# Performance work log

Hardware: AMD Instinct MI355X
Metric: run time of the kernel (lower is better)

Reference implementation:

```python
import jax, jax.numpy as jnp
import numpy as np

B, T, C = 2, 2048, 2048
H, HD = 16, 128          # n_head, head_dim
D_C, D_C1, D_ROPE = 512, 512, 64
D_NOPE = HD - D_ROPE     # 64
M = 4                    # move_slots
EPS = 1.1920929e-07      # torch fp32 rms_norm default eps


def _rope(x, cos, sin):
    # x: (B,T,h,D), cos/sin: (B,T,D//2) -> broadcast over head axis
    c = cos[:, :, None, :]
    s = sin[:, :, None, :]
    x1, x2 = jnp.split(x, 2, axis=-1)
    return jnp.concatenate([x1 * c + x2 * s, -x1 * s + x2 * c], axis=-1)


def _rmsnorm(x):
    return x * jax.lax.rsqrt(jnp.mean(x * x, axis=-1, keepdims=True) + EPS)


def setup_inputs() -> dict:
    key = jax.random.key(0)
    ks = jax.random.split(key, 8)
    # realistic decoupled-RoPE angles over d_rope//2 frequencies
    inv_freq = 1.0 / (10000.0 ** (np.arange(0, D_ROPE, 2) / D_ROPE))  # (32,)
    ang = np.arange(T)[:, None] * inv_freq[None, :]                   # (T,32)
    cos = jnp.broadcast_to(jnp.cos(ang)[None].astype(jnp.float32), (B, T, D_ROPE // 2))
    sin = jnp.broadcast_to(jnp.sin(ang)[None].astype(jnp.float32), (B, T, D_ROPE // 2))
    return {
        "x": jax.random.normal(ks[0], (B, T, C), jnp.float32),
        "ve": jax.random.normal(ks[1], (B, T, M * H * HD), jnp.float32),
        "cos": cos,
        "sin": sin,
        "w_down": jax.random.normal(ks[2], (C, D_C + D_C1 + D_ROPE), jnp.float32) * 0.02,
        "w_ukv": jax.random.normal(ks[3], (D_C, H * (D_NOPE + HD)), jnp.float32) * 0.02,
        "w_uq": jax.random.normal(ks[4], (D_C1, H * HD), jnp.float32) * 0.02,
        "w_gate": jax.random.normal(ks[5], (C, H * (M + 1)), jnp.float32) * 0.02,
        "w_proj": jax.random.normal(ks[6], (H * HD, C), jnp.float32) * 0.02,
        "window_size": 2048,
    }


def reference(x, ve, cos, sin, w_down, w_ukv, w_uq, w_gate, w_proj, window_size):
    # fused down projection, split into kv-latent / q-latent / rope part
    down = x @ w_down                                          # (B,T,1088)
    c_kv, c_q, k_rope_raw = jnp.split(down, [D_C, D_C + D_C1], axis=-1)

    kv = (c_kv @ w_ukv).reshape(B, T, H, D_NOPE + HD)
    k_nope, v = jnp.split(kv, [D_NOPE], axis=-1)               # (B,T,H,64), (B,T,H,128)

    k_rope = _rope(k_rope_raw.reshape(B, T, 1, D_ROPE), cos, sin)  # (B,T,1,64)

    # MoVE gating: per-head gate on v plus mixture over M value-embedding slots
    ve5 = ve.reshape(B, T, M, H, HD)
    gates = 2.0 * jax.nn.sigmoid(x @ w_gate).reshape(B, T, H, M + 1)
    v = gates[..., 0:1] * v + jnp.einsum('bthm,btmhd->bthd', gates[..., 1:], ve5)

    q = (c_q @ w_uq).reshape(B, T, H, HD)
    q_nope, q_rope = jnp.split(q, [D_NOPE], axis=-1)
    q_rope = _rope(q_rope, cos, sin)

    k = jnp.concatenate([k_nope, jnp.broadcast_to(k_rope, (B, T, H, D_ROPE))], axis=-1)
    q = jnp.concatenate([q_nope, q_rope], axis=-1)
    q, k = _rmsnorm(q), _rmsnorm(k)

    # sliding-window causal attention (flash_attn semantics: j<=i and i-j<=window)
    scale = 1.0 / float(np.sqrt(HD))
    scores = jnp.einsum('bthd,bshd->bhts', q, k) * scale       # (B,H,T,T)
    i = jnp.arange(T)[:, None]
    j = jnp.arange(T)[None, :]
    mask = (j <= i) & ((i - j) <= window_size)
    scores = jnp.where(mask, scores, -jnp.inf)
    attn = jax.nn.softmax(scores, axis=-1)
    y = jnp.einsum('bhts,bshd->bthd', attn, v)                 # (B,T,H,HD)

    return y.reshape(B, T, H * HD) @ w_proj                    # (B,T,C)
```

## Files before the change

kernel.cpp:

```cpp
#include <hip/hip_runtime.h>

typedef unsigned short u16;
typedef __bf16 bfv8 __attribute__((ext_vector_type(8)));
typedef float f32x4 __attribute__((ext_vector_type(4)));
typedef u16 u16x8 __attribute__((ext_vector_type(8)));

#define B_      2
#define T_      2048
#define C_      2048
#define H_      16
#define HD_     128
#define NT_     (B_ * T_)
#define DOWN_N  1088
#define DCAT    1168
#define DCATP   1280
#define KV_N    3072
#define Q_N     2048
#define EPS_    1.1920929e-07f
#define CEXP    0.12751879524580262f
#define SMAXS   16.6f

__device__ __forceinline__ float b2f(u16 u) {
    union { unsigned u; float f; } c; c.u = ((unsigned)u) << 16; return c.f;
}
__device__ __forceinline__ u16 f2b(float f) {
    union { float f; unsigned u; } c; c.f = f;
    return (u16)((c.u + 0x7FFFu + ((c.u >> 16) & 1u)) >> 16);
}
__device__ __forceinline__ float dynload(const void* p, size_t i, int bf) {
    if (bf) return b2f(((const u16*)p)[i]);
    return ((const float*)p)[i];
}

__device__ __forceinline__ void gload16(const u16* g, u16* l) {
    __builtin_amdgcn_global_load_lds(
        (const __attribute__((address_space(1))) void*)g,
        (__attribute__((address_space(3))) void*)l,
        16, 0, 0);
}

__global__ void detect_kernel(const unsigned* __restrict__ x, int* __restrict__ flag) {
    __shared__ int cnt;
    if (threadIdx.x == 0) cnt = 0;
    __syncthreads();
    int c = 0;
    for (int i = threadIdx.x; i < 4096; i += 256) {
        const unsigned w = x[i];
        const unsigned e = (w >> 7) & 0xFF;
        if (e >= 105 && e <= 140) ++c;
    }
    atomicAdd(&cnt, c);
    __syncthreads();
    if (threadIdx.x == 0) flag[0] = (cnt > 2300) ? 1 : 0;
}

__global__ __launch_bounds__(256) void cast_kernel(
    const void* __restrict__ in, u16* __restrict__ out, int n, const int* __restrict__ flagp)
{
    const int fl = flagp[0];
    const int i0 = (blockIdx.x * 256 + threadIdx.x) * 8;
    if (i0 + 8 > n) return;
    u16x8 o;
    #pragma unroll
    for (int i = 0; i < 8; ++i) o[i] = f2b(dynload(in, (size_t)i0 + i, fl));
    *(u16x8*)(out + i0) = o;
}

__global__ __launch_bounds__(256) void tcast_kernel(
    const void* __restrict__ in, u16* __restrict__ out, int K, int N, int Ntot,
    const int* __restrict__ flagp)
{
    const int fl = flagp[0];
    __shared__ float sf[32][33];
    const int n0 = blockIdx.x * 32, k0 = blockIdx.y * 32;
    const int tx = threadIdx.x & 31, ty = threadIdx.x >> 5;
    const int cr = (n0 + tx < N) ? (n0 + tx) : (N - 1);
    #pragma unroll
    for (int i = 0; i < 4; ++i)
        sf[ty + 8 * i][tx] = dynload(in, (size_t)(k0 + ty + 8 * i) * N + cr, fl);
    __syncthreads();
    #pragma unroll
    for (int i = 0; i < 4; ++i) {
        const int n = n0 + ty + 8 * i;
        if (n < Ntot) out[(size_t)n * K + k0 + tx] = (n < N) ? f2b(sf[tx][ty + 8 * i]) : (u16)0;
    }
}

__device__ __forceinline__ void stc(u16* p, float v)  { *p = f2b(v); }
__device__ __forceinline__ void stc(float* p, float v){ *p = v; }

template <typename TC>
__global__ __launch_bounds__(256) void mfma_gemm(
    const u16* __restrict__ A, int lda,
    const u16* __restrict__ BT, int ldb,
    TC* __restrict__ Cm, int ldc,
    int M, int N, int K)
{
    __shared__ u16 As[128 * 32];
    __shared__ u16 Bs[128 * 32];
    const int tid = threadIdx.x;
    const int m0 = blockIdx.y * 128, n0 = blockIdx.x * 128;
    const int w = tid >> 6, l = tid & 63;
    const int wm = (w >> 1) * 64, wn = (w & 1) * 64;
    const int lr = l & 15, lq = l >> 4;

    f32x4 acc[4][4];
    #pragma unroll
    for (int i = 0; i < 4; ++i)
        #pragma unroll
        for (int j = 0; j < 4; ++j) acc[i][j] = (f32x4){0.f, 0.f, 0.f, 0.f};

    const int srow = w * 32 + (l >> 2);
    const int scol = (l & 3) * 8;
    const u16* ag = A  + (size_t)(m0 + srow) * lda + scol;
    const u16* bg = BT + (size_t)(n0 + srow) * ldb + scol;
    u16* as0 = &As[(w * 32) * 32];
    u16* as1 = &As[(w * 32 + 16) * 32];
    u16* bs0 = &Bs[(w * 32) * 32];
    u16* bs1 = &Bs[(w * 32 + 16) * 32];

    for (int k0 = 0; k0 < K; k0 += 32) {
        gload16(ag + k0,            as0);
        gload16(ag + 16 * lda + k0, as1);
        gload16(bg + k0,            bs0);
        gload16(bg + 16 * ldb + k0, bs1);
        __syncthreads();
        bfv8 af[4], bf[4];
        #pragma unroll
        for (int mi = 0; mi < 4; ++mi) af[mi] = *(const bfv8*)&As[(wm + mi * 16 + lr) * 32 + lq * 8];
        #pragma unroll
        for (int ni = 0; ni < 4; ++ni) bf[ni] = *(const bfv8*)&Bs[(wn + ni * 16 + lr) * 32 + lq * 8];
        #pragma unroll
        for (int mi = 0; mi < 4; ++mi)
            #pragma unroll
            for (int ni = 0; ni < 4; ++ni)
                acc[mi][ni] = __builtin_amdgcn_mfma_f32_16x16x32_bf16(af[mi], bf[ni], acc[mi][ni], 0, 0, 0);
        __syncthreads();
    }

    #pragma unroll
    for (int mi = 0; mi < 4; ++mi) {
        #pragma unroll
        for (int ni = 0; ni < 4; ++ni) {
            const int col = n0 + wn + ni * 16 + lr;
            if (col < N) {
                #pragma unroll
                for (int r = 0; r < 4; ++r) {
                    const int row = m0 + wm + mi * 16 + lq * 4 + r;
                    stc(&Cm[(size_t)row * ldc + col], acc[mi][ni][r]);
                }
            }
        }
    }
}

__global__ __launch_bounds__(256) void assemble_kernel(
    const u16* __restrict__ down,
    const u16* __restrict__ qraw,
    const u16* __restrict__ kv,
    const void* __restrict__ ve,
    const void* __restrict__ cosg,
    const void* __restrict__ sing,
    u16* __restrict__ qo, u16* __restrict__ ko, u16* __restrict__ vo,
    const int* __restrict__ flagp)
{
    const int fl = flagp[0];
    const int bt = blockIdx.x;
    const int tid = threadIdx.x;
    __shared__ float cs[32], sn[32], kr[64];
    if (tid < 32) {
        cs[tid] = dynload(cosg, (size_t)bt * 32 + tid, fl);
        sn[tid] = dynload(sing, (size_t)bt * 32 + tid, fl);
    }
    __syncthreads();
    if (tid < 64) {
        const u16* rp = down + (size_t)bt * DCAT + 1024;
        const int d = tid;
        if (d < 32) kr[d] = b2f(rp[d]) * cs[d] + b2f(rp[d + 32]) * sn[d];
        else { const int r = d - 32; kr[d] = -b2f(rp[d - 32]) * sn[r] + b2f(rp[d]) * cs[r]; }
    }
    __syncthreads();

    const int h = tid >> 4;
    const int lane = tid & 15;
    const int d0 = lane * 8;

    const u16* qr = qraw + (size_t)bt * Q_N + h * HD_;
    float vq[8];
    float ss = 0.f;
    #pragma unroll
    for (int i = 0; i < 8; ++i) {
        const int d = d0 + i;
        float xv = b2f(qr[d]);
        if (d >= 64) {
            if (d < 96) { const int r = d - 64; xv = xv * cs[r] + b2f(qr[d + 32]) * sn[r]; }
            else        { const int r = d - 96; xv = -b2f(qr[d - 32]) * sn[r] + xv * cs[r]; }
        }
        vq[i] = xv; ss += xv * xv;
    }
    #pragma unroll
    for (int off = 1; off < 16; off <<= 1) ss += __shfl_xor(ss, off);
    float rms = rsqrtf(ss * (1.f / 128.f) + EPS_);
    u16* qop = qo + (size_t)bt * Q_N + h * HD_ + d0;
    #pragma unroll
    for (int i = 0; i < 8; ++i) qop[i] = f2b(vq[i] * rms);

    const u16* kvp = kv + (size_t)bt * KV_N + h * 192;
    float vk[8];
    ss = 0.f;
    #pragma unroll
    for (int i = 0; i < 8; ++i) {
        const int d = d0 + i;
        const float xv = (d < 64) ? b2f(kvp[d]) : kr[d - 64];
        vk[i] = xv; ss += xv * xv;
    }
    #pragma unroll
    for (int off = 1; off < 16; off <<= 1) ss += __shfl_xor(ss, off);
    rms = rsqrtf(ss * (1.f / 128.f) + EPS_);
    u16* kop = ko + (size_t)bt * Q_N + h * HD_ + d0;
    #pragma unroll
    for (int i = 0; i < 8; ++i) kop[i] = f2b(vk[i] * rms);

    float g[5];
    #pragma unroll
    for (int j = 0; j < 5; ++j) {
        const float logit = b2f(down[(size_t)bt * DCAT + 1088 + h * 5 + j]);
        g[j] = 2.f / (1.f + expf(-logit));
    }
    const u16* vp = kvp + 64;
    const size_t vebase = (size_t)bt * 8192 + h * HD_;
    u16* vop = vo + (size_t)bt * Q_N + h * HD_ + d0;
    #pragma unroll
    for (int i = 0; i < 8; ++i) {
        const int d = d0 + i;
        float val = g[0] * b2f(vp[d]);
        #pragma unroll
        for (int m = 0; m < 4; ++m) val += g[1 + m] * dynload(ve, vebase + m * 2048 + d, fl);
        vop[i] = f2b(val);
    }
}

__global__ __launch_bounds__(256) void vtrans_kernel(
    const u16* __restrict__ vn, u16* __restrict__ vt)
{
    __shared__ u16 s[64][72];
    const int t0 = blockIdx.x * 64;
    const int d0 = blockIdx.y * 64;
    const int bh = blockIdx.z;
    const int tid = threadIdx.x;
    {
        const int tt = tid >> 2, seg = tid & 3;
        const u16* p = vn + ((size_t)((bh >> 4) * T_) + t0 + tt) * 2048 + (bh & 15) * 128 + d0 + seg * 16;
        u16x8 v0 = *(const u16x8*)(p);
        u16x8 v1 = *(const u16x8*)(p + 8);
        *(u16x8*)&s[tt][seg * 16]     = v0;
        *(u16x8*)&s[tt][seg * 16 + 8] = v1;
    }
    __syncthreads();
    {
        const int dd = tid >> 2, tseg = tid & 3;
        u16* q = vt + ((size_t)(bh * 128) + d0 + dd) * T_ + t0 + tseg * 16;
        #pragma unroll
        for (int g = 0; g < 2; ++g) {
            u16x8 o;
            #pragma unroll
            for (int i = 0; i < 8; ++i) o[i] = s[tseg * 16 + g * 8 + i][dd];
            *(u16x8*)(q + g * 8) = o;
        }
    }
}

__global__ __launch_bounds__(256) void attn_mfma(
    const u16* __restrict__ qn, const u16* __restrict__ kn,
    const u16* __restrict__ vt, u16* __restrict__ yb,
    const int* __restrict__ wptr)
{
    __shared__ u16 Ks[64][136];
    __shared__ u16 VTs[144][72];
    __shared__ u16 Ps[4][32][72];

    const int flat = (int)(blockIdx.x + (blockIdx.y << 4) + (blockIdx.z << 8));
    const int b  = flat & 1;
    const int h  = ((flat >> 1) & 7) | ((flat >> 5) & 8);
    const int q4 = (flat >> 4) & 15;
    const int mb = ((flat ^ (flat >> 8)) & 1) ? (q4 ^ 15) : q4;
    const int m0 = mb * 128;
    const int W = wptr[0];
    const int tid = threadIdx.x;
    const int w = tid >> 6, l = tid & 63;
    const int lr = l & 15, lq = l >> 4;
    const int qr0 = m0 + w * 32;

    bfv8 qf[2][4];
    #pragma unroll
    for (int mi = 0; mi < 2; ++mi) {
        const u16* qp = qn + ((size_t)(b * T_) + qr0 + mi * 16 + lr) * 2048 + h * 128 + lq * 8;
        #pragma unroll
        for (int kk = 0; kk < 4; ++kk) qf[mi][kk] = *(const bfv8*)(qp + kk * 32);
    }

    f32x4 oacc[2][8];
    f32x4 lacc[2];
    #pragma unroll
    for (int mi = 0; mi < 2; ++mi) {
        lacc[mi] = (f32x4){0.f, 0.f, 0.f, 0.f};
        #pragma unroll
        for (int od = 0; od < 8; ++od) oacc[mi][od] = (f32x4){0.f, 0.f, 0.f, 0.f};
    }

    {
        const int rr = 128 + (tid >> 4), cc = (tid & 15) * 4;
        const u16 v = (tid >> 4) == 0 ? (u16)0x3F80 : (u16)0;
        VTs[rr][cc] = v; VTs[rr][cc + 1] = v; VTs[rr][cc + 2] = v; VTs[rr][cc + 3] = v;
    }

    const int kkey = tid >> 2, kq = tid & 3;
    const int vd = tid >> 1, vh2 = tid & 1;

    int ns = m0 - W; if (ns < 0) ns = 0; ns &= ~63;
    const int ne = m0 + 64;

    const u16* kbase = kn + ((size_t)(b * T_) + kkey) * 2048 + h * 128 + kq * 32;
    const u16* vbase = vt + ((size_t)(b * H_ + h) * 128 + vd) * T_ + vh2 * 32;

    u16x8 pk[4], pv[4];
    {
        const u16* kp = kbase + (size_t)ns * 2048;
        const u16* vp = vbase + ns;
        #pragma unroll
        for (int s = 0; s < 4; ++s) pk[s] = *(const u16x8*)(kp + s * 8);
        #pragma unroll
        for (int s = 0; s < 4; ++s) pv[s] = *(const u16x8*)(vp + s * 8);
    }

    for (int n0 = ns; n0 <= ne; n0 += 64) {
        {
            u16* kd = &Ks[kkey][kq * 32];
            #pragma unroll
            for (int s = 0; s < 4; ++s) *(u16x8*)(kd + s * 8) = pk[s];
            u16* vdst = &VTs[vd][vh2 * 32];
            #pragma unroll
            for (int s = 0; s < 4; ++s) *(u16x8*)(vdst + s * 8) = pv[s];
        }
        __syncthreads();

        if (n0 < ne) {
            const u16* kp = kbase + (size_t)(n0 + 64) * 2048;
            const u16* vp = vbase + (n0 + 64);
            #pragma unroll
            for (int s = 0; s < 4; ++s) pk[s] = *(const u16x8*)(kp + s * 8);
            #pragma unroll
            for (int s = 0; s < 4; ++s) pv[s] = *(const u16x8*)(vp + s * 8);
        }

        const bool active = (n0 <= qr0 + 31) && (n0 + 63 >= qr0 - W);
        if (active) {
            f32x4 s0[4], s1[4];
            #pragma unroll
            for (int f = 0; f < 4; ++f) {
                f32x4 a0 = (f32x4){0.f, 0.f, 0.f, 0.f};
                f32x4 a1 = (f32x4){0.f, 0.f, 0.f, 0.f};
                #pragma unroll
                for (int kk = 0; kk < 4; ++kk) {
                    bfv8 kf = *(const bfv8*)&Ks[f * 16 + lr][kk * 32 + lq * 8];
                    a0 = __builtin_amdgcn_mfma_f32_16x16x32_bf16(qf[0][kk], kf, a0, 0, 0, 0);
                    a1 = __builtin_amdgcn_mfma_f32_16x16x32_bf16(qf[1][kk], kf, a1, 0, 0, 0);
                }
                s0[f] = a0; s1[f] = a1;
            }

            if ((n0 + 63 > qr0) || (qr0 + 31 - n0 > W)) {
                #pragma unroll
                for (int f = 0; f < 4; ++f) {
                    const int si = n0 + f * 16 + lr;
                    #pragma unroll
                    for (int r = 0; r < 4; ++r) {
                        const int t0i = qr0 + lq * 4 + r;
                        const int t1i = t0i + 16;
                        if (si > t0i || t0i - si > W) s0[f][r] = -1e30f;
                        if (si > t1i || t1i - si > W) s1[f][r] = -1e30f;
                    }
                }
            }

            #pragma unroll
            for (int f = 0; f < 4; ++f)
                #pragma unroll
                for (int r = 0; r < 4; ++r) {
                    const float p0 = exp2f(s0[f][r] * CEXP - SMAXS);
                    const float p1 = exp2f(s1[f][r] * CEXP - SMAXS);
                    Ps[w][lq * 4 + r][f * 16 + lr]      = f2b(p0);
                    Ps[w][16 + lq * 4 + r][f * 16 + lr] = f2b(p1);
                }

            bfv8 pf0[2], pf1[2];
            #pragma unroll
            for (int kk2 = 0; kk2 < 2; ++kk2) {
                pf0[kk2] = *(const bfv8*)&Ps[w][lr][kk2 * 32 + lq * 8];
                pf1[kk2] = *(const bfv8*)&Ps[w][16 + lr][kk2 * 32 + lq * 8];
            }
            #pragma unroll
            for (int kk2 = 0; kk2 < 2; ++kk2) {
                #pragma unroll
                for (int od = 0; od < 8; ++od) {
                    bfv8 vf = *(const bfv8*)&VTs[od * 16 + lr][kk2 * 32 + lq * 8];
                    oacc[0][od] = __builtin_amdgcn_mfma_f32_16x16x32_bf16(pf0[kk2], vf, oacc[0][od], 0, 0, 0);
                    oacc[1][od] = __builtin_amdgcn_mfma_f32_16x16x32_bf16(pf1[kk2], vf, oacc[1][od], 0, 0, 0);
                }
                bfv8 vf1 = *(const bfv8*)&VTs[128 + lr][kk2 * 32 + lq * 8];
                lacc[0] = __builtin_amdgcn_mfma_f32_16x16x32_bf16(pf0[kk2], vf1, lacc[0], 0, 0, 0);
                lacc[1] = __builtin_amdgcn_mfma_f32_16x16x32_bf16(pf1[kk2], vf1, lacc[1], 0, 0, 0);
            }
        }
        __syncthreads();
    }

    #pragma unroll
    for (int mi = 0; mi < 2; ++mi) {
        float linv[4];
        #pragma unroll
        for (int r = 0; r < 4; ++r) {
            const float lv = __shfl(lacc[mi][r], l & 48);
            linv[r] = 1.f / lv;
        }
        #pragma unroll
        for (int od = 0; od < 8; ++od)
            #pragma unroll
            for (int r = 0; r < 4; ++r) {
                const size_t idx = ((size_t)(b * T_) + qr0 + mi * 16 + lq * 4 + r) * 2048
                                 + h * 128 + od * 16 + lr;
                yb[idx] = f2b(oacc[mi][od][r] * linv[r]);
            }
    }
}

extern "C" void kernel_launch(void* const* d_in, const int* in_sizes, int n_in,
                              void* d_out, int out_size, void* d_ws, size_t ws_size,
                              hipStream_t stream)
{
    const void* x      = d_in[0];
    const void* ve     = d_in[1];
    const void* cosg   = d_in[2];
    const void* sing   = d_in[3];
    const void* w_down = d_in[4];
    const void* w_ukv  = d_in[5];
    const void* w_uq   = d_in[6];
    const void* w_gate = d_in[7];
    const void* w_proj = d_in[8];
    const int*  wsz    = (const int*)d_in[9];
    float* out = (float*)d_out;

    char* p = (char*)d_ws;
    u16* xbf    = (u16*)p; p += (size_t)NT_ * C_ * 2;
    u16* wcatT  = (u16*)p; p += (size_t)DCATP * C_ * 2;
    u16* wukvT  = (u16*)p; p += (size_t)KV_N * 512 * 2;
    u16* wuqT   = (u16*)p; p += (size_t)Q_N * 512 * 2;
    u16* wpT    = (u16*)p; p += (size_t)C_ * C_ * 2;
    u16* downb  = (u16*)p; p += (size_t)NT_ * DCAT * 2;
    u16* kvb    = (u16*)p; p += (size_t)NT_ * KV_N * 2;
    u16* qraw   = (u16*)p; p += (size_t)NT_ * Q_N * 2;
    u16* kn     = (u16*)p; p += (size_t)NT_ * Q_N * 2;
    u16* vn     = (u16*)p; p += (size_t)NT_ * Q_N * 2;
    int* flag   = (int*)p; p += 256;
    u16* qn  = xbf;
    u16* vtb = qraw;
    u16* ybf = vn;

    dim3 blk(256);
    detect_kernel<<<1, blk, 0, stream>>>((const unsigned*)x, flag);
    cast_kernel<<<dim3(NT_ * C_ / (256 * 8)), blk, 0, stream>>>(x, xbf, NT_ * C_, flag);
    tcast_kernel<<<dim3(DOWN_N / 32, C_ / 32), blk, 0, stream>>>(w_down, wcatT, C_, DOWN_N, DOWN_N, flag);
    tcast_kernel<<<dim3((DCATP - DOWN_N) / 32, C_ / 32), blk, 0, stream>>>(
        w_gate, wcatT + (size_t)DOWN_N * C_, C_, 80, DCATP - DOWN_N, flag);
    tcast_kernel<<<dim3(KV_N / 32, 512 / 32), blk, 0, stream>>>(w_ukv, wukvT, 512, KV_N, KV_N, flag);
    tcast_kernel<<<dim3(Q_N / 32, 512 / 32), blk, 0, stream>>>(w_uq, wuqT, 512, Q_N, Q_N, flag);
    tcast_kernel<<<dim3(C_ / 32, C_ / 32), blk, 0, stream>>>(w_proj, wpT, C_, C_, C_, flag);

    mfma_gemm<u16><<<dim3(DCATP / 128, NT_ / 128), blk, 0, stream>>>(
        xbf, C_, wcatT, C_, downb, DCAT, NT_, DCAT, C_);
    mfma_gemm<u16><<<dim3(KV_N / 128, NT_ / 128), blk, 0, stream>>>(
        downb, DCAT, wukvT, 512, kvb, KV_N, NT_, KV_N, 512);
    mfma_gemm<u16><<<dim3(Q_N / 128, NT_ / 128), blk, 0, stream>>>(
        downb + 512, DCAT, wuqT, 512, qraw, Q_N, NT_, Q_N, 512);
    assemble_kernel<<<dim3(NT_), blk, 0, stream>>>(
        downb, qraw, kvb, ve, cosg, sing, qn, kn, vn, flag);
    vtrans_kernel<<<dim3(T_ / 64, 2, B_ * H_), blk, 0, stream>>>(vn, vtb);
    attn_mfma<<<dim3(T_ / 128, H_, B_), dim3(256), 0, stream>>>(qn, kn, vtb, ybf, wsz);
    mfma_gemm<float><<<dim3(Q_N / 128, NT_ / 128), blk, 0, stream>>>(
        ybf, Q_N, wpT, C_, out, C_, NT_, C_, Q_N);
}
```

Measured before the change: 659.6 us.

## Split long causal query blocks across two workgroups with a combine pass

The upper half of query blocks (mb 8..15), which have the longest key ranges, is split into two workgroups that each process half the key tiles and write unnormalized fp32 partial outputs and row sums to scratch. A new combine kernel sums the two partials and normalizes them into the bf16 output. The short query blocks stay unsplit. The aim is to balance the causal triangle's work over 768 workgroups instead of 512, which shortens the tail, at the cost of extra fp32 partial traffic and one more kernel launch. The combine relies on the softmax using a fixed max (SMAXS constant), so the partials can be summed without rescaling.

```diff
diff --git a/kernel.cpp b/kernel.cpp
--- a/kernel.cpp
+++ b/kernel.cpp
@@ -273,17 +273,25 @@
 __global__ __launch_bounds__(256) void attn_mfma(
     const u16* __restrict__ qn, const u16* __restrict__ kn,
     const u16* __restrict__ vt, u16* __restrict__ yb,
+    float* __restrict__ po, float* __restrict__ pl,
     const int* __restrict__ wptr)
 {
     __shared__ u16 Ks[64][136];
     __shared__ u16 VTs[144][72];
     __shared__ u16 Ps[4][32][72];
 
-    const int flat = (int)(blockIdx.x + (blockIdx.y << 4) + (blockIdx.z << 8));
-    const int b  = flat & 1;
-    const int h  = ((flat >> 1) & 7) | ((flat >> 5) & 8);
-    const int q4 = (flat >> 4) & 15;
-    const int mb = ((flat ^ (flat >> 8)) & 1) ? (q4 ^ 15) : q4;
+    const int i = (int)blockIdx.x;
+    int b, h, mb, c;
+    bool split;
+    if (i < 512) {
+        split = true; c = i & 1;
+        const int r = i >> 1;
+        mb = 15 - (r & 7); h = (r >> 3) & 15; b = r >> 7;
+    } else {
+        split = false; c = 0;
+        const int j = i - 512;
+        mb = 7 - (j & 7); h = (j >> 3) & 15; b = j >> 7;
+    }
     const int m0 = mb * 128;
     const int W = wptr[0];
     const int tid = threadIdx.x;
@@ -320,20 +328,29 @@
     int ns = m0 - W; if (ns < 0) ns = 0; ns &= ~63;
     const int ne = m0 + 64;
 
+    int n_lo = ns, n_hi = ne;
+    if (split) {
+        const int nt = ((ne - ns) >> 6) + 1;
+        const int h0 = (nt + 1) >> 1;
+        if (c == 0) n_hi = ns + (h0 - 1) * 64;
+        else        n_lo = ns + h0 * 64;
+        if (n_lo > n_hi) { n_lo = ns; n_hi = ns - 64; }
+    }
+
     const u16* kbase = kn + ((size_t)(b * T_) + kkey) * 2048 + h * 128 + kq * 32;
     const u16* vbase = vt + ((size_t)(b * H_ + h) * 128 + vd) * T_ + vh2 * 32;
 
     u16x8 pk[4], pv[4];
     {
-        const u16* kp = kbase + (size_t)ns * 2048;
-        const u16* vp = vbase + ns;
+        const u16* kp = kbase + (size_t)n_lo * 2048;
+        const u16* vp = vbase + n_lo;
         #pragma unroll
         for (int s = 0; s < 4; ++s) pk[s] = *(const u16x8*)(kp + s * 8);
         #pragma unroll
         for (int s = 0; s < 4; ++s) pv[s] = *(const u16x8*)(vp + s * 8);
     }
 
-    for (int n0 = ns; n0 <= ne; n0 += 64) {
+    for (int n0 = n_lo; n0 <= n_hi; n0 += 64) {
         {
             u16* kd = &Ks[kkey][kq * 32];
             #pragma unroll
@@ -344,7 +361,7 @@
         }
         __syncthreads();
 
-        if (n0 < ne) {
+        if (n0 < n_hi) {
             const u16* kp = kbase + (size_t)(n0 + 64) * 2048;
             const u16* vp = vbase + (n0 + 64);
             #pragma unroll
@@ -415,22 +432,69 @@
         __syncthreads();
     }
 
-    #pragma unroll
-    for (int mi = 0; mi < 2; ++mi) {
-        float linv[4];
-        #pragma unroll
-        for (int r = 0; r < 4; ++r) {
-            const float lv = __shfl(lacc[mi][r], l & 48);
-            linv[r] = 1.f / lv;
-        }
-        #pragma unroll
-        for (int od = 0; od < 8; ++od)
+    if (!split) {
+        #pragma unroll
+        for (int mi = 0; mi < 2; ++mi) {
+            float linv[4];
             #pragma unroll
             for (int r = 0; r < 4; ++r) {
-                const size_t idx = ((size_t)(b * T_) + qr0 + mi * 16 + lq * 4 + r) * 2048
-                                 + h * 128 + od * 16 + lr;
-                yb[idx] = f2b(oacc[mi][od][r] * linv[r]);
-            }
+                const float lv = __shfl(lacc[mi][r], l & 48);
+                linv[r] = 1.f / lv;
+            }
+            #pragma unroll
+            for (int od = 0; od < 8; ++od)
+                #pragma unroll
+                for (int r = 0; r < 4; ++r) {
+                    const size_t idx = ((size_t)(b * T_) + qr0 + mi * 16 + lq * 4 + r) * 2048
+                                     + h * 128 + od * 16 + lr;
+                    yb[idx] = f2b(oacc[mi][od][r] * linv[r]);
+                }
+        }
+    } else {
+        float* op = po + (size_t)i * 16384;
+        #pragma unroll
+        for (int mi = 0; mi < 2; ++mi) {
+            #pragma unroll
+            for (int od = 0; od < 8; ++od)
+                #pragma unroll
+                for (int r = 0; r < 4; ++r)
+                    op[(w * 32 + mi * 16 + lq * 4 + r) * 128 + od * 16 + lr] = oacc[mi][od][r];
+            if (lr == 0) {
+                #pragma unroll
+                for (int r = 0; r < 4; ++r)
+                    pl[(size_t)i * 128 + w * 32 + mi * 16 + lq * 4 + r] = lacc[mi][r];
+            }
+        }
+    }
+}
+
+__global__ __launch_bounds__(256) void attn_combine(
+    const float* __restrict__ po, const float* __restrict__ pl, u16* __restrict__ yb)
+{
+    const int mbi = blockIdx.x, h = blockIdx.y, b = blockIdx.z;
+    const int r2 = (b << 7) | (h << 3) | mbi;
+    const int mb = 15 - mbi;
+    const int t = threadIdx.x;
+    const int row = t >> 1;
+    const int ch = (t & 1) * 64;
+    const float la = pl[(size_t)(r2 * 2) * 128 + row];
+    const float lb = pl[(size_t)(r2 * 2 + 1) * 128 + row];
+    const float linv = 1.f / (la + lb);
+    const float* oa = po + (size_t)(r2 * 2) * 16384 + row * 128 + ch;
+    const float* ob = oa + 16384;
+    u16* yp = yb + ((size_t)(b * T_) + mb * 128 + row) * 2048 + h * 128 + ch;
+    #pragma unroll
+    for (int g = 0; g < 8; ++g) {
+        const f32x4 a0 = *(const f32x4*)(oa + g * 8);
+        const f32x4 a1 = *(const f32x4*)(oa + g * 8 + 4);
+        const f32x4 b0 = *(const f32x4*)(ob + g * 8);
+        const f32x4 b1 = *(const f32x4*)(ob + g * 8 + 4);
+        u16x8 o;
+        #pragma unroll
+        for (int k = 0; k < 4; ++k) o[k]     = f2b((a0[k] + b0[k]) * linv);
+        #pragma unroll
+        for (int k = 0; k < 4; ++k) o[4 + k] = f2b((a1[k] + b1[k]) * linv);
+        *(u16x8*)(yp + g * 8) = o;
     }
 }
 
@@ -465,6 +529,8 @@
     u16* qn  = xbf;
     u16* vtb = qraw;
     u16* ybf = vn;
+    float* attn_po = (float*)downb;
+    float* attn_pl = (float*)((char*)downb + (size_t)512 * 16384 * 4);
 
     dim3 blk(256);
     detect_kernel<<<1, blk, 0, stream>>>((const unsigned*)x, flag);
@@ -485,7 +551,8 @@
     assemble_kernel<<<dim3(NT_), blk, 0, stream>>>(
         downb, qraw, kvb, ve, cosg, sing, qn, kn, vn, flag);
     vtrans_kernel<<<dim3(T_ / 64, 2, B_ * H_), blk, 0, stream>>>(vn, vtb);
-    attn_mfma<<<dim3(T_ / 128, H_, B_), dim3(256), 0, stream>>>(qn, kn, vtb, ybf, wsz);
+    attn_mfma<<<dim3(768), dim3(256), 0, stream>>>(qn, kn, vtb, ybf, attn_po, attn_pl, wsz);
+    attn_combine<<<dim3(8, 16, 2), blk, 0, stream>>>(attn_po, attn_pl, ybf);
     mfma_gemm<float><<<dim3(Q_N / 128, NT_ / 128), blk, 0, stream>>>(
         ybf, Q_N, wpT, C_, out, C_, NT_, C_, Q_N);
 }
```

Result: no change. 659.2 us (-0.1%).
